# Kernel optimization log

Hardware: AMD Instinct MI355X
Metric: run time of the kernel (lower is better)

## Reference

```python
import jax, jax.numpy as jnp
import numpy as np

D_MODEL = 2048
EXPAND = 2
INNER = EXPAND * D_MODEL          # 4096
HEADDIM = 64
NHEADS = INNER // HEADDIM         # 64
D_CONV = 4
BATCH, SEQLEN = 2, 4096


def setup_inputs() -> dict:
    key = jax.random.key(0)
    ks = jax.random.split(key, 12)
    f32 = jnp.float32
    return {
        "hidden_states": jax.random.normal(ks[0], (BATCH, SEQLEN, D_MODEL), f32),
        "in_proj_w": jax.random.normal(ks[1], (INNER, D_MODEL), f32) * 0.02,
        "gate_proj_w": jax.random.normal(ks[2], (INNER, D_MODEL), f32) * 0.02,
        "out_proj_w": jax.random.normal(ks[3], (D_MODEL, INNER), f32) * 0.02,
        "conv_weight": jax.random.normal(ks[4], (INNER, D_CONV), f32) * 0.02,
        "conv_bias": jnp.zeros((INNER,), f32),
        "dt_w": jax.random.normal(ks[5], (NHEADS, HEADDIM), f32) * 0.02,
        "dt_b": jnp.zeros((NHEADS,), f32),
        "A_log": jax.random.normal(ks[6], (NHEADS, HEADDIM), f32) * 0.1,
        "B": jax.random.normal(ks[7], (NHEADS, HEADDIM), f32) * 0.02,
        "C": jax.random.normal(ks[8], (NHEADS, HEADDIM), f32) * 0.02,
        "D": jnp.ones((NHEADS, HEADDIM), f32),
    }


def _dw_causal_conv_silu(x, w, b):
    # x: (B, L, C), w: (C, K), b: (C,). Causal depthwise conv + SiLU.
    K = w.shape[1]
    L = x.shape[1]
    xp = jnp.pad(x, ((0, 0), (K - 1, 0), (0, 0)))
    y = b
    for k in range(K):  # K=4, tiny fixed loop
        y = y + w[:, k] * xp[:, k:k + L, :]
    return jax.nn.silu(y)


def _diag_ssm_scan(a, u):
    # Linear recurrence s_t = a_t * s_{t-1} + u_t along axis=1 (seqlen).
    def comb(c1, c2):
        a1, b1 = c1
        a2, b2 = c2
        return a1 * a2, a2 * b1 + b2
    _, s = jax.lax.associative_scan(comb, (a, u), axis=1)
    return s


def reference(hidden_states, in_proj_w, gate_proj_w, out_proj_w,
              conv_weight, conv_bias, dt_w, dt_b, A_log, B, C, D):
    batch, seqlen, _ = hidden_states.shape
    projected = jnp.einsum('bld,cd->blc', hidden_states, in_proj_w)
    conv_out = _dw_causal_conv_silu(projected, conv_weight, conv_bias)
    gate = jax.nn.sigmoid(jnp.einsum('bld,cd->blc', hidden_states, gate_proj_w))

    X = conv_out.reshape(batch, seqlen, NHEADS, HEADDIM)
    dt = jax.nn.softplus(jnp.einsum('blhp,hp->blh', X, dt_w) + dt_b)  # (b,l,h)
    A = -jnp.exp(A_log)                                               # (h,p)

    a = jnp.exp(dt[..., None] * A)          # (b,l,h,p) decay factors
    u = dt[..., None] * B * X               # (b,l,h,p) driven input
    s = _diag_ssm_scan(a, u)                # (b,l,h,p) states
    y = C * s + D * X                       # (b,l,h,p)

    combined = y.reshape(batch, seqlen, INNER) * gate
    return jnp.einsum('blc,dc->bld', combined, out_proj_w)
```

## Files before the change

kernel.cpp:

```cpp
#include <hip/hip_runtime.h>
#include <cstdint>
#include <cstddef>

typedef unsigned short ushort;
typedef unsigned int uint;
typedef __attribute__((ext_vector_type(8))) short short8;
typedef __attribute__((ext_vector_type(8))) unsigned short ushort8;
typedef __attribute__((ext_vector_type(4))) float float4v;

#define DM    2048
#define INNERC 4096
#define LSEQ  4096
#define NBATCH 2
#define MROWS 8192
#define NHH   64
#define HDD   64
#define NCHUNK 32
#define CHLEN  128

__device__ __forceinline__ float bf2f(ushort u) {
    return __uint_as_float(((unsigned int)u) << 16);
}
__device__ __forceinline__ ushort f2bf(float f) {
    unsigned int u = __float_as_uint(f);
    unsigned int r = u + 0x7FFFu + ((u >> 16) & 1u);
    return (ushort)(r >> 16);
}

__device__ __forceinline__ void async_cp16(const ushort* __restrict__ g, ushort* l) {
    __builtin_amdgcn_global_load_lds(
        (const __attribute__((address_space(1))) unsigned int*)g,
        (__attribute__((address_space(3))) unsigned int*)l,
        16, 0, 0);
}

__global__ void diag_kernel(float* __restrict__ out, float val) {
    if (threadIdx.x == 0 && blockIdx.x == 0) out[0] = val;
}

__global__ __launch_bounds__(256) void cast_bf16_kernel(
    const float* __restrict__ in, ushort* __restrict__ out, int n) {
    const int i = (blockIdx.x * 256 + threadIdx.x) * 8;
    if (i + 8 > n) return;
    const float4v a = *(const float4v*)(in + i);
    const float4v b = *(const float4v*)(in + i + 4);
    ushort8 o;
    o[0] = f2bf(a[0]); o[1] = f2bf(a[1]); o[2] = f2bf(a[2]); o[3] = f2bf(a[3]);
    o[4] = f2bf(b[0]); o[5] = f2bf(b[1]); o[6] = f2bf(b[2]); o[7] = f2bf(b[3]);
    *(ushort8*)(out + i) = o;
}

__global__ __launch_bounds__(256) void cast2_bf16_kernel(
    const float* __restrict__ in1, ushort* __restrict__ out1, int n1,
    const float* __restrict__ in2, ushort* __restrict__ out2, int n2) {
    int i = (blockIdx.x * 256 + threadIdx.x) * 8;
    const float* in;
    ushort* out;
    if (i < n1) {
        in = in1 + i; out = out1 + i;
    } else {
        const int j = i - n1;
        if (j + 8 > n2) return;
        in = in2 + j; out = out2 + j;
    }
    const float4v a = *(const float4v*)(in);
    const float4v b = *(const float4v*)(in + 4);
    ushort8 o;
    o[0] = f2bf(a[0]); o[1] = f2bf(a[1]); o[2] = f2bf(a[2]); o[3] = f2bf(a[3]);
    o[4] = f2bf(b[0]); o[5] = f2bf(b[1]); o[6] = f2bf(b[2]); o[7] = f2bf(b[3]);
    *(ushort8*)(out) = o;
}


#define PH_PRE() __builtin_amdgcn_s_barrier()
#define PH_POST() __builtin_amdgcn_s_barrier()

#define MFMA_Q(AF, RBASE, CL) do { \
    __builtin_amdgcn_s_setprio(1); \
    _Pragma("unroll") for (int kk = 0; kk < 2; ++kk) \
    _Pragma("unroll") for (int rm = 0; rm < 4; ++rm) \
    _Pragma("unroll") for (int cn = 0; cn < 2; ++cn) \
        acc[(RBASE) + rm][(CL) + cn] = __builtin_amdgcn_mfma_f32_16x16x32_bf16( \
            AF[rm][kk], bf[(CL) + cn][kk], acc[(RBASE) + rm][(CL) + cn], 0, 0, 0); \
    __builtin_amdgcn_s_setprio(0); } while (0)

#define READ_A(DST, BUF, HB) do { \
    _Pragma("unroll") for (int rm = 0; rm < 4; ++rm) { \
        DST[rm][0] = *(const short8*)&As[BUF][offA_k0 + ((HB) * 4 + rm) * 1024]; \
        DST[rm][1] = *(const short8*)&As[BUF][offA_k1 + ((HB) * 4 + rm) * 1024]; \
    } } while (0)

#define READ_B2(BUF, CNLO) do { \
    _Pragma("unroll") for (int cn = 0; cn < 2; ++cn) { \
        bf[(CNLO) + cn][0] = *(const short8*)&Bs[BUF][offB_k0 + ((CNLO) + cn) * 1024]; \
        bf[(CNLO) + cn][1] = *(const short8*)&Bs[BUF][offB_k1 + ((CNLO) + cn) * 1024]; \
    } } while (0)

#define STAGE(G, OFF, LBASE) do { \
    async_cp16((G) + (OFF),       (LBASE) + (tid << 3)); \
    async_cp16((G) + (OFF) + k64, (LBASE) + (tid << 3) + 4096); \
    (OFF) += 64; } while (0)

template <int EPI>
__global__ __launch_bounds__(512, 2) void gemm256(
    const ushort* __restrict__ Ab, const ushort* __restrict__ Wb,
    void* __restrict__ Out, const ushort* __restrict__ Aux,
    int M, int N, int K) {
    __shared__ ushort As[2][16384];
    __shared__ ushort Bs[2][16384];

    const int tid  = threadIdx.x;
    const int lane = tid & 63;
    const int w    = tid >> 6;
    const int wm   = w >> 2;
    const int wn   = w & 3;
    const int l15  = lane & 15;
    const int l4   = lane >> 4;
    const int swz7 = l15 & 7;
    const int s01  = swz7 & 3;
    const int b2   = (swz7 >> 2) & 1;

    const int gx   = gridDim.x;
    const int nwg  = gx * gridDim.y;
    const int orig = blockIdx.y * gx + blockIdx.x;
    const int swz  = (orig & 7) * (nwg >> 3) + (orig >> 3);
    const int row0 = (swz / gx) * 256;
    const int col0 = (swz % gx) * 256;

    const int ni = K >> 7;

    const int commA   = (wm * 128 + l15) * 64 + (l4 ^ s01) * 8;
    const int offA_k0 = commA + (b2 ? 32 : 0);
    const int offA_k1 = commA + (b2 ? 0 : 32);
    const int commB   = (wn * 64 + l15) * 64 + (l4 ^ s01) * 8;
    const int offB_k0 = commB + (b2 ? 32 : 0);
    const int offB_k1 = commB + (b2 ? 0 : 32);

    const uint rr8 = (uint)(tid >> 3);
    const uint kg8 = (uint)(((tid & 7) ^ ((tid >> 3) & 7)) * 8);
    const uint k64 = (uint)64 * (uint)K;
    uint oA0 = (uint)(row0) * (uint)K + rr8 * (uint)K + kg8;
    uint oA1 = oA0 + (uint)128 * (uint)K;
    uint oW0 = (uint)(col0) * (uint)K + rr8 * (uint)K + kg8;
    uint oW1 = oW0 + (uint)128 * (uint)K;

    float4v acc[8][4];
#pragma unroll
    for (int i2 = 0; i2 < 8; i2++)
#pragma unroll
        for (int j2 = 0; j2 < 4; j2++) {
            float4v z = {0.f, 0.f, 0.f, 0.f};
            acc[i2][j2] = z;
        }

    short8 afL[4][2], afH[4][2], bf[4][2];

    STAGE(Ab, oA0, &As[0][0]);
    STAGE(Ab, oA1, &As[0][8192]);
    STAGE(Wb, oW0, &Bs[0][0]);
    STAGE(Wb, oW1, &Bs[0][8192]);
    STAGE(Ab, oA0, &As[1][0]);
    STAGE(Ab, oA1, &As[1][8192]);
    STAGE(Wb, oW0, &Bs[1][0]);
    STAGE(Wb, oW1, &Bs[1][8192]);
    asm volatile("s_waitcnt vmcnt(8)" ::: "memory");
    __builtin_amdgcn_s_barrier();

#pragma unroll 1
    for (int i = 0; i < ni - 1; ++i) {
        READ_A(afL, 0, 0);
        READ_B2(0, 0);
        asm volatile("s_waitcnt lgkmcnt(8)");
        PH_PRE();
        MFMA_Q(afL, 0, 0);
        PH_POST();

        READ_B2(0, 2);
        PH_PRE();
        MFMA_Q(afL, 0, 2);
        PH_POST();

        READ_A(afH, 0, 1);
        STAGE(Wb, oW0, &Bs[0][0]);
        PH_PRE();
        MFMA_Q(afH, 4, 2);
        PH_POST();

        STAGE(Wb, oW1, &Bs[0][8192]);
        PH_PRE();
        MFMA_Q(afH, 4, 0);
        asm volatile("s_waitcnt vmcnt(4)" ::: "memory");
        __builtin_amdgcn_s_barrier();

        READ_A(afL, 1, 0);
        READ_B2(1, 0);
        STAGE(Ab, oA0, &As[0][0]);
        asm volatile("s_waitcnt lgkmcnt(8)");
        PH_PRE();
        MFMA_Q(afL, 0, 0);
        PH_POST();

        READ_B2(1, 2);
        STAGE(Ab, oA1, &As[0][8192]);
        PH_PRE();
        MFMA_Q(afL, 0, 2);
        PH_POST();

        READ_A(afH, 1, 1);
        STAGE(Wb, oW0, &Bs[1][0]);
        STAGE(Wb, oW1, &Bs[1][8192]);
        PH_PRE();
        MFMA_Q(afH, 4, 2);
        PH_POST();

        STAGE(Ab, oA0, &As[1][0]);
        STAGE(Ab, oA1, &As[1][8192]);
        PH_PRE();
        MFMA_Q(afH, 4, 0);
        asm volatile("s_waitcnt vmcnt(8)" ::: "memory");
        __builtin_amdgcn_s_barrier();
    }

    {
        READ_A(afL, 0, 0);
        READ_B2(0, 0);
        READ_B2(0, 2);
        READ_A(afH, 0, 1);
        __builtin_amdgcn_s_setprio(1);
        MFMA_Q(afL, 0, 0);
        MFMA_Q(afL, 0, 2);
        MFMA_Q(afH, 4, 2);
        MFMA_Q(afH, 4, 0);
        __builtin_amdgcn_s_setprio(0);
        asm volatile("s_waitcnt vmcnt(0)" ::: "memory");
        __builtin_amdgcn_s_barrier();
        READ_A(afL, 1, 0);
        READ_B2(1, 0);
        READ_B2(1, 2);
        READ_A(afH, 1, 1);
        __builtin_amdgcn_s_setprio(1);
        MFMA_Q(afL, 0, 0);
        MFMA_Q(afL, 0, 2);
        MFMA_Q(afH, 4, 2);
        MFMA_Q(afH, 4, 0);
        __builtin_amdgcn_s_setprio(0);
    }

#pragma unroll
    for (int rm = 0; rm < 8; ++rm) {
#pragma unroll
        for (int cn = 0; cn < 4; ++cn) {
            const int r0 = row0 + wm * 128 + rm * 16 + l4 * 4;
            const int cc = col0 + wn * 64 + cn * 16 + l15;
#pragma unroll
            for (int rr = 0; rr < 4; ++rr) {
                const float v = acc[rm][cn][rr];
                const size_t off = (size_t)(r0 + rr) * N + cc;
                if (EPI == 0) {
                    ((ushort*)Out)[off] = f2bf(v);
                } else if (EPI == 1) {
                    const float g = 1.0f / (1.0f + __expf(-v));
                    ((ushort*)Out)[off] = f2bf(g * bf2f(Aux[off]));
                } else {
                    ((float*)Out)[off] = v;
                }
            }
        }
    }
}

#define CSCH 256
__global__ __launch_bounds__(256) void conv_scan1_kernel(
    const ushort* __restrict__ proj, const float* __restrict__ cw,
    const float* __restrict__ cb, const float* __restrict__ dtw,
    const float* __restrict__ dtb, const float* __restrict__ A_log,
    const float* __restrict__ Bv, ushort* __restrict__ X,
    float* __restrict__ dt, float* __restrict__ sumP,
    float* __restrict__ sumS) {
    const int blk   = blockIdx.x;
    const int slice = blk & 15;
    const int chunk = blk >> 4;
    const int b     = chunk >> 5;
    const int chk   = chunk & 31;
    const int bl0   = b * LSEQ + chk * CHLEN;
    const int c     = slice * CSCH + threadIdx.x;
    const int h     = c >> 6;
    const int p     = c & 63;
    const int lane  = threadIdx.x & 63;

    const float4v wv   = *(const float4v*)(cw + (size_t)c * 4);
    const float biasv  = cb[c];
    const float dtwv   = dtw[c];
    const float dtbv   = dtb[h];
    const float Ac     = -__expf(A_log[c]);
    const float Bc     = Bv[c];

    const size_t base = (size_t)bl0 * INNERC + c;
    float f0, f1, f2;
    if (chk == 0) {
        f0 = 0.f; f1 = 0.f; f2 = 0.f;
    } else {
        f0 = bf2f(proj[base - 3 * (size_t)INNERC]);
        f1 = bf2f(proj[base - 2 * (size_t)INNERC]);
        f2 = bf2f(proj[base - 1 * (size_t)INNERC]);
    }

    float Pr = 1.0f, s = 0.0f;
#pragma unroll 4
    for (int r = 0; r < CHLEN; ++r) {
        const float fc = bf2f(proj[base + (size_t)r * INNERC]);
        const float a4 = biasv + wv[0] * f0 + wv[1] * f1 + wv[2] * f2 + wv[3] * fc;
        const float sl = a4 / (1.0f + __expf(-a4));
        const ushort xb = f2bf(sl);
        X[base + (size_t)r * INNERC] = xb;
        float d = sl * dtwv;
        d += __shfl_xor(d, 1, 64);
        d += __shfl_xor(d, 2, 64);
        d += __shfl_xor(d, 4, 64);
        d += __shfl_xor(d, 8, 64);
        d += __shfl_xor(d, 16, 64);
        d += __shfl_xor(d, 32, 64);
        const float z   = d + dtbv;
        const float dtv = (z > 20.0f) ? z : __logf(1.0f + __expf(z));
        if (lane == 0) dt[(bl0 + r) * 64 + h] = dtv;
        const float xr = bf2f(xb);
        const float aa = __expf(dtv * Ac);
        Pr *= aa;
        s = aa * s + dtv * Bc * xr;
        f0 = f1; f1 = f2; f2 = fc;
    }
    const size_t task = (size_t)((b * 64 + h) * 32 + chk);
    sumP[task * 64 + p] = Pr;
    sumS[task * 64 + p] = s;
}

__global__ __launch_bounds__(64) void scan_pass2(
    const float* __restrict__ sumP, const float* __restrict__ sumS,
    float* __restrict__ carry) {
    const int bh = blockIdx.x;
    const int p  = threadIdx.x;
    float c = 0.0f;
    for (int ch = 0; ch < NCHUNK; ch++) {
        const size_t idx = ((size_t)bh * NCHUNK + ch) * 64 + p;
        carry[idx] = c;
        c = sumP[idx] * c + sumS[idx];
    }
}

__global__ __launch_bounds__(256) void scan_pass3(
    const ushort* __restrict__ X, const float* __restrict__ dt,
    const float* __restrict__ carry,
    const float* __restrict__ A_log, const float* __restrict__ Bv,
    const float* __restrict__ Cv, const float* __restrict__ Dv,
    ushort* __restrict__ Y) {
    const int task = blockIdx.x * 4 + (threadIdx.x >> 6);
    const int p  = threadIdx.x & 63;
    const int ch = task & (NCHUNK - 1);
    const int bh = task >> 5;
    const int h  = bh & 63;
    const int b  = bh >> 6;
    const float Ac = -__expf(A_log[h * 64 + p]);
    const float Bc = Bv[h * 64 + p];
    const float Cc = Cv[h * 64 + p];
    const float Dc = Dv[h * 64 + p];
    float s = carry[(size_t)task * 64 + p];
    const int bl0 = b * LSEQ + ch * CHLEN;
#pragma unroll 2
    for (int i = 0; i < CHLEN; i++) {
        const int bl = bl0 + i;
        const size_t xoff = (size_t)bl * INNERC + h * 64 + p;
        const float dtv = dt[bl * 64 + h];
        const float x   = bf2f(X[xoff]);
        const float a   = __expf(dtv * Ac);
        s = a * s + dtv * Bc * x;
        Y[xoff] = f2bf(Cc * s + Dc * x);
    }
}

#define OFF_PROJ  ((size_t)0)
#define OFF_HID   ((size_t)67108864)
#define OFF_WB    ((size_t)100663296)
#define OFF_DT    ((size_t)117440512)
#define OFF_SUMP  ((size_t)119537664)
#define OFF_SUMS  ((size_t)120586240)
#define OFF_CARRY ((size_t)121634816)
#define WS_NEEDED ((size_t)122683392)

extern "C" void kernel_launch(void* const* d_in, const int* in_sizes, int n_in,
                              void* d_out, int out_size, void* d_ws, size_t ws_size,
                              hipStream_t stream) {
    if (ws_size < WS_NEEDED) {
        diag_kernel<<<1, 64, 0, stream>>>((float*)d_out, (float)(ws_size >> 20));
        return;
    }
    const float* hidden = (const float*)d_in[0];
    const float* w_in   = (const float*)d_in[1];
    const float* w_gate = (const float*)d_in[2];
    const float* w_out  = (const float*)d_in[3];
    const float* conv_w = (const float*)d_in[4];
    const float* conv_b = (const float*)d_in[5];
    const float* dt_w   = (const float*)d_in[6];
    const float* dt_b   = (const float*)d_in[7];
    const float* A_log  = (const float*)d_in[8];
    const float* Bv     = (const float*)d_in[9];
    const float* Cv     = (const float*)d_in[10];
    const float* Dv     = (const float*)d_in[11];

    char* ws = (char*)d_ws;
    ushort* projbuf = (ushort*)(ws + OFF_PROJ);
    ushort* hid16   = (ushort*)(ws + OFF_HID);
    ushort* wbuf    = (ushort*)(ws + OFF_WB);
    float*  dtf     = (float*)(ws + OFF_DT);
    float*  sumP    = (float*)(ws + OFF_SUMP);
    float*  sumS    = (float*)(ws + OFF_SUMS);
    float*  carry   = (float*)(ws + OFF_CARRY);
    ushort* x16     = (ushort*)d_out;

    cast2_bf16_kernel<<<12288, 256, 0, stream>>>(
        hidden, hid16, MROWS * DM, w_in, wbuf, INNERC * DM);

    gemm256<0><<<dim3(INNERC / 256, MROWS / 256), 512, 0, stream>>>(
        hid16, wbuf, projbuf, nullptr, MROWS, INNERC, DM);

    conv_scan1_kernel<<<(INNERC / CSCH) * (NBATCH * NCHUNK), 256, 0, stream>>>(
        projbuf, conv_w, conv_b, dt_w, dt_b, A_log, Bv, x16, dtf, sumP, sumS);

    scan_pass2<<<NBATCH * NHH, 64, 0, stream>>>(sumP, sumS, carry);
    scan_pass3<<<(NBATCH * NHH * NCHUNK) / 4, 256, 0, stream>>>(
        x16, dtf, carry, A_log, Bv, Cv, Dv, projbuf);

    cast_bf16_kernel<<<4096, 256, 0, stream>>>(w_gate, wbuf, INNERC * DM);
    gemm256<1><<<dim3(INNERC / 256, MROWS / 256), 512, 0, stream>>>(
        hid16, wbuf, projbuf, projbuf, MROWS, INNERC, DM);

    cast_bf16_kernel<<<4096, 256, 0, stream>>>(w_out, wbuf, DM * INNERC);
    gemm256<2><<<dim3(DM / 256, MROWS / 256), 512, 0, stream>>>(
        projbuf, wbuf, d_out, nullptr, MROWS, DM, INNERC);
}
```

Before: 695.4 us.

## Recompute conv in scan pass, fold carry propagation, fuse gate weight cast

Splits the conv+SSM work into two passes that each recompute the causal conv and dt from the projection. The X and dt intermediates are no longer written, and the separate carry kernel is removed because each chunk replays the prefix of chunk summaries itself. Each thread now handles four channels with vectorized loads, and the gate-weight bf16 cast rides along as extra blocks in the first pass. This saves memory traffic and launches at the cost of doing the conv/dt arithmetic twice, plus a serial carry loop of up to 31 chunks per thread.

```diff
diff --git a/kernel.cpp b/kernel.cpp
--- a/kernel.cpp
+++ b/kernel.cpp
@@ -6,6 +6,7 @@
 typedef unsigned int uint;
 typedef __attribute__((ext_vector_type(8))) short short8;
 typedef __attribute__((ext_vector_type(8))) unsigned short ushort8;
+typedef __attribute__((ext_vector_type(4))) unsigned short us4;
 typedef __attribute__((ext_vector_type(4))) float float4v;
 
 #define DM    2048
@@ -17,6 +18,7 @@
 #define HDD   64
 #define NCHUNK 32
 #define CHLEN  128
+#define NSCAN  512
 
 __device__ __forceinline__ float bf2f(ushort u) {
     return __uint_as_float(((unsigned int)u) << 16);
@@ -269,111 +271,181 @@
     }
 }
 
-#define CSCH 256
-__global__ __launch_bounds__(256) void conv_scan1_kernel(
+
+__device__ __forceinline__ void conv_row_setup(
+    const float* __restrict__ cw, const float* __restrict__ cb,
+    const float* __restrict__ dtw, int c0,
+    float4v w[4], float4v* bias, float4v* dtwv) {
+    const float4v* wp = (const float4v*)(cw + (size_t)c0 * 4);
+#pragma unroll
+    for (int j = 0; j < 4; ++j) w[j] = wp[j];
+    *bias = *(const float4v*)(cb + c0);
+    *dtwv = *(const float4v*)(dtw + c0);
+}
+
+__device__ __forceinline__ float conv_row(
+    const us4 cur, float4v* f0, float4v* f1, float4v* f2,
+    const float4v w[4], const float4v bias, const float4v dtwv,
+    const float dtbv, float sl[4]) {
+    float4v fc;
+#pragma unroll
+    for (int j = 0; j < 4; ++j) fc[j] = bf2f(cur[j]);
+    float d = 0.0f;
+#pragma unroll
+    for (int j = 0; j < 4; ++j) {
+        const float a4 = bias[j] + w[j][0] * (*f0)[j] + w[j][1] * (*f1)[j]
+                       + w[j][2] * (*f2)[j] + w[j][3] * fc[j];
+        const float s = a4 / (1.0f + __expf(-a4));
+        sl[j] = s;
+        d += s * dtwv[j];
+    }
+    *f0 = *f1; *f1 = *f2; *f2 = fc;
+    d += __shfl_xor(d, 1, 64);
+    d += __shfl_xor(d, 2, 64);
+    d += __shfl_xor(d, 4, 64);
+    d += __shfl_xor(d, 8, 64);
+    const float z = d + dtbv;
+    return (z > 20.0f) ? z : __logf(1.0f + __expf(z));
+}
+
+__global__ __launch_bounds__(128) void conv_scanA(
     const ushort* __restrict__ proj, const float* __restrict__ cw,
     const float* __restrict__ cb, const float* __restrict__ dtw,
     const float* __restrict__ dtb, const float* __restrict__ A_log,
-    const float* __restrict__ Bv, ushort* __restrict__ X,
-    float* __restrict__ dt, float* __restrict__ sumP,
-    float* __restrict__ sumS) {
-    const int blk   = blockIdx.x;
-    const int slice = blk & 15;
-    const int chunk = blk >> 4;
-    const int b     = chunk >> 5;
-    const int chk   = chunk & 31;
+    const float* __restrict__ Bv, float* __restrict__ sumP,
+    float* __restrict__ sumS,
+    const float* __restrict__ wg, ushort* __restrict__ wgb) {
+    const int bid = blockIdx.x;
+    if (bid >= NSCAN) {
+        const int i = (bid - NSCAN) * 1024 + threadIdx.x * 8;
+        const float4v a = *(const float4v*)(wg + i);
+        const float4v b = *(const float4v*)(wg + i + 4);
+        ushort8 o;
+        o[0] = f2bf(a[0]); o[1] = f2bf(a[1]); o[2] = f2bf(a[2]); o[3] = f2bf(a[3]);
+        o[4] = f2bf(b[0]); o[5] = f2bf(b[1]); o[6] = f2bf(b[2]); o[7] = f2bf(b[3]);
+        *(ushort8*)(wgb + i) = o;
+        return;
+    }
+    const int slice = bid & 7;
+    const int chk   = (bid >> 3) & 31;
+    const int b     = bid >> 8;
+    const int tid   = threadIdx.x;
+    const int c0    = slice * 512 + tid * 4;
+    const int h     = c0 >> 6;
     const int bl0   = b * LSEQ + chk * CHLEN;
-    const int c     = slice * CSCH + threadIdx.x;
-    const int h     = c >> 6;
-    const int p     = c & 63;
-    const int lane  = threadIdx.x & 63;
-
-    const float4v wv   = *(const float4v*)(cw + (size_t)c * 4);
-    const float biasv  = cb[c];
-    const float dtwv   = dtw[c];
-    const float dtbv   = dtb[h];
-    const float Ac     = -__expf(A_log[c]);
-    const float Bc     = Bv[c];
-
-    const size_t base = (size_t)bl0 * INNERC + c;
-    float f0, f1, f2;
+
+    float4v w[4], bias, dtwv;
+    conv_row_setup(cw, cb, dtw, c0, w, &bias, &dtwv);
+    const float dtbv = dtb[h];
+    const float4v Alv = *(const float4v*)(A_log + c0);
+    const float4v Bc  = *(const float4v*)(Bv + c0);
+    float Ac[4];
+#pragma unroll
+    for (int j = 0; j < 4; ++j) Ac[j] = -__expf(Alv[j]);
+
+    const size_t base = (size_t)bl0 * INNERC + c0;
+    float4v f0, f1, f2;
     if (chk == 0) {
-        f0 = 0.f; f1 = 0.f; f2 = 0.f;
+#pragma unroll
+        for (int j = 0; j < 4; ++j) { f0[j] = 0.f; f1[j] = 0.f; f2[j] = 0.f; }
     } else {
-        f0 = bf2f(proj[base - 3 * (size_t)INNERC]);
-        f1 = bf2f(proj[base - 2 * (size_t)INNERC]);
-        f2 = bf2f(proj[base - 1 * (size_t)INNERC]);
-    }
-
-    float Pr = 1.0f, s = 0.0f;
+        const us4 u0 = *(const us4*)(proj + base - 3 * (size_t)INNERC);
+        const us4 u1 = *(const us4*)(proj + base - 2 * (size_t)INNERC);
+        const us4 u2 = *(const us4*)(proj + base - 1 * (size_t)INNERC);
+#pragma unroll
+        for (int j = 0; j < 4; ++j) {
+            f0[j] = bf2f(u0[j]); f1[j] = bf2f(u1[j]); f2[j] = bf2f(u2[j]);
+        }
+    }
+
+    float4v Pr, sv;
+#pragma unroll
+    for (int j = 0; j < 4; ++j) { Pr[j] = 1.0f; sv[j] = 0.0f; }
 #pragma unroll 4
     for (int r = 0; r < CHLEN; ++r) {
-        const float fc = bf2f(proj[base + (size_t)r * INNERC]);
-        const float a4 = biasv + wv[0] * f0 + wv[1] * f1 + wv[2] * f2 + wv[3] * fc;
-        const float sl = a4 / (1.0f + __expf(-a4));
-        const ushort xb = f2bf(sl);
-        X[base + (size_t)r * INNERC] = xb;
-        float d = sl * dtwv;
-        d += __shfl_xor(d, 1, 64);
-        d += __shfl_xor(d, 2, 64);
-        d += __shfl_xor(d, 4, 64);
-        d += __shfl_xor(d, 8, 64);
-        d += __shfl_xor(d, 16, 64);
-        d += __shfl_xor(d, 32, 64);
-        const float z   = d + dtbv;
-        const float dtv = (z > 20.0f) ? z : __logf(1.0f + __expf(z));
-        if (lane == 0) dt[(bl0 + r) * 64 + h] = dtv;
-        const float xr = bf2f(xb);
-        const float aa = __expf(dtv * Ac);
-        Pr *= aa;
-        s = aa * s + dtv * Bc * xr;
-        f0 = f1; f1 = f2; f2 = fc;
+        const us4 cur = *(const us4*)(proj + base + (size_t)r * INNERC);
+        float sl[4];
+        const float dtv = conv_row(cur, &f0, &f1, &f2, w, bias, dtwv, dtbv, sl);
+#pragma unroll
+        for (int j = 0; j < 4; ++j) {
+            const float aa = __expf(dtv * Ac[j]);
+            Pr[j] *= aa;
+            sv[j] = aa * sv[j] + dtv * Bc[j] * sl[j];
+        }
     }
     const size_t task = (size_t)((b * 64 + h) * 32 + chk);
-    sumP[task * 64 + p] = Pr;
-    sumS[task * 64 + p] = s;
-}
-
-__global__ __launch_bounds__(64) void scan_pass2(
-    const float* __restrict__ sumP, const float* __restrict__ sumS,
-    float* __restrict__ carry) {
-    const int bh = blockIdx.x;
-    const int p  = threadIdx.x;
-    float c = 0.0f;
-    for (int ch = 0; ch < NCHUNK; ch++) {
-        const size_t idx = ((size_t)bh * NCHUNK + ch) * 64 + p;
-        carry[idx] = c;
-        c = sumP[idx] * c + sumS[idx];
-    }
-}
-
-__global__ __launch_bounds__(256) void scan_pass3(
-    const ushort* __restrict__ X, const float* __restrict__ dt,
-    const float* __restrict__ carry,
-    const float* __restrict__ A_log, const float* __restrict__ Bv,
-    const float* __restrict__ Cv, const float* __restrict__ Dv,
-    ushort* __restrict__ Y) {
-    const int task = blockIdx.x * 4 + (threadIdx.x >> 6);
-    const int p  = threadIdx.x & 63;
-    const int ch = task & (NCHUNK - 1);
-    const int bh = task >> 5;
-    const int h  = bh & 63;
-    const int b  = bh >> 6;
-    const float Ac = -__expf(A_log[h * 64 + p]);
-    const float Bc = Bv[h * 64 + p];
-    const float Cc = Cv[h * 64 + p];
-    const float Dc = Dv[h * 64 + p];
-    float s = carry[(size_t)task * 64 + p];
-    const int bl0 = b * LSEQ + ch * CHLEN;
-#pragma unroll 2
-    for (int i = 0; i < CHLEN; i++) {
-        const int bl = bl0 + i;
-        const size_t xoff = (size_t)bl * INNERC + h * 64 + p;
-        const float dtv = dt[bl * 64 + h];
-        const float x   = bf2f(X[xoff]);
-        const float a   = __expf(dtv * Ac);
-        s = a * s + dtv * Bc * x;
-        Y[xoff] = f2bf(Cc * s + Dc * x);
+    const int p4 = (tid & 15) * 4;
+    *(float4v*)(sumP + task * 64 + p4) = Pr;
+    *(float4v*)(sumS + task * 64 + p4) = sv;
+}
+
+__global__ __launch_bounds__(128) void conv_scanB(
+    const ushort* __restrict__ proj, const float* __restrict__ cw,
+    const float* __restrict__ cb, const float* __restrict__ dtw,
+    const float* __restrict__ dtb, const float* __restrict__ A_log,
+    const float* __restrict__ Bv, const float* __restrict__ Cv,
+    const float* __restrict__ Dv, const float* __restrict__ sumP,
+    const float* __restrict__ sumS, ushort* __restrict__ Y) {
+    const int bid   = blockIdx.x;
+    const int slice = bid & 7;
+    const int chk   = (bid >> 3) & 31;
+    const int b     = bid >> 8;
+    const int tid   = threadIdx.x;
+    const int c0    = slice * 512 + tid * 4;
+    const int h     = c0 >> 6;
+    const int bl0   = b * LSEQ + chk * CHLEN;
+
+    float4v w[4], bias, dtwv;
+    conv_row_setup(cw, cb, dtw, c0, w, &bias, &dtwv);
+    const float dtbv = dtb[h];
+    const float4v Alv = *(const float4v*)(A_log + c0);
+    const float4v Bc  = *(const float4v*)(Bv + c0);
+    const float4v Cc  = *(const float4v*)(Cv + c0);
+    const float4v Dc  = *(const float4v*)(Dv + c0);
+    float Ac[4];
+#pragma unroll
+    for (int j = 0; j < 4; ++j) Ac[j] = -__expf(Alv[j]);
+
+    const int p4 = (tid & 15) * 4;
+    const size_t bh32 = (size_t)(b * 64 + h) * 32;
+    float4v sv;
+#pragma unroll
+    for (int j = 0; j < 4; ++j) sv[j] = 0.0f;
+    for (int jc = 0; jc < chk; ++jc) {
+        const float4v P = *(const float4v*)(sumP + (bh32 + jc) * 64 + p4);
+        const float4v S = *(const float4v*)(sumS + (bh32 + jc) * 64 + p4);
+#pragma unroll
+        for (int j = 0; j < 4; ++j) sv[j] = P[j] * sv[j] + S[j];
+    }
+
+    const size_t base = (size_t)bl0 * INNERC + c0;
+    float4v f0, f1, f2;
+    if (chk == 0) {
+#pragma unroll
+        for (int j = 0; j < 4; ++j) { f0[j] = 0.f; f1[j] = 0.f; f2[j] = 0.f; }
+    } else {
+        const us4 u0 = *(const us4*)(proj + base - 3 * (size_t)INNERC);
+        const us4 u1 = *(const us4*)(proj + base - 2 * (size_t)INNERC);
+        const us4 u2 = *(const us4*)(proj + base - 1 * (size_t)INNERC);
+#pragma unroll
+        for (int j = 0; j < 4; ++j) {
+            f0[j] = bf2f(u0[j]); f1[j] = bf2f(u1[j]); f2[j] = bf2f(u2[j]);
+        }
+    }
+
+#pragma unroll 4
+    for (int r = 0; r < CHLEN; ++r) {
+        const us4 cur = *(const us4*)(proj + base + (size_t)r * INNERC);
+        float sl[4];
+        const float dtv = conv_row(cur, &f0, &f1, &f2, w, bias, dtwv, dtbv, sl);
+        us4 yo;
+#pragma unroll
+        for (int j = 0; j < 4; ++j) {
+            const float aa = __expf(dtv * Ac[j]);
+            sv[j] = aa * sv[j] + dtv * Bc[j] * sl[j];
+            yo[j] = f2bf(Cc[j] * sv[j] + Dc[j] * sl[j]);
+        }
+        *(us4*)(Y + base + (size_t)r * INNERC) = yo;
     }
 }
 
@@ -410,11 +482,9 @@
     ushort* projbuf = (ushort*)(ws + OFF_PROJ);
     ushort* hid16   = (ushort*)(ws + OFF_HID);
     ushort* wbuf    = (ushort*)(ws + OFF_WB);
-    float*  dtf     = (float*)(ws + OFF_DT);
     float*  sumP    = (float*)(ws + OFF_SUMP);
     float*  sumS    = (float*)(ws + OFF_SUMS);
-    float*  carry   = (float*)(ws + OFF_CARRY);
-    ushort* x16     = (ushort*)d_out;
+    ushort* y16     = (ushort*)d_out;
 
     cast2_bf16_kernel<<<12288, 256, 0, stream>>>(
         hidden, hid16, MROWS * DM, w_in, wbuf, INNERC * DM);
@@ -422,16 +492,16 @@
     gemm256<0><<<dim3(INNERC / 256, MROWS / 256), 512, 0, stream>>>(
         hid16, wbuf, projbuf, nullptr, MROWS, INNERC, DM);
 
-    conv_scan1_kernel<<<(INNERC / CSCH) * (NBATCH * NCHUNK), 256, 0, stream>>>(
-        projbuf, conv_w, conv_b, dt_w, dt_b, A_log, Bv, x16, dtf, sumP, sumS);
-
-    scan_pass2<<<NBATCH * NHH, 64, 0, stream>>>(sumP, sumS, carry);
-    scan_pass3<<<(NBATCH * NHH * NCHUNK) / 4, 256, 0, stream>>>(
-        x16, dtf, carry, A_log, Bv, Cv, Dv, projbuf);
-
-    cast_bf16_kernel<<<4096, 256, 0, stream>>>(w_gate, wbuf, INNERC * DM);
+    conv_scanA<<<NSCAN + 8192, 128, 0, stream>>>(
+        projbuf, conv_w, conv_b, dt_w, dt_b, A_log, Bv, sumP, sumS,
+        w_gate, wbuf);
+
+    conv_scanB<<<NSCAN, 128, 0, stream>>>(
+        projbuf, conv_w, conv_b, dt_w, dt_b, A_log, Bv, Cv, Dv,
+        sumP, sumS, y16);
+
     gemm256<1><<<dim3(INNERC / 256, MROWS / 256), 512, 0, stream>>>(
-        hid16, wbuf, projbuf, projbuf, MROWS, INNERC, DM);
+        hid16, wbuf, projbuf, y16, MROWS, INNERC, DM);
 
     cast_bf16_kernel<<<4096, 256, 0, stream>>>(w_out, wbuf, DM * INNERC);
     gemm256<2><<<dim3(DM / 256, MROWS / 256), 512, 0, stream>>>(
```

Result: no change. 699.9 us (+0.6%).
